# Kernel optimization log

Measured on AMD Instinct MI355X. Metric: run time of the kernel, lower is better.

Reference implementation:

```python
import jax, jax.numpy as jnp
import numpy as np

T, B, D, E, H = 64, 1024, 128, 256, 512


def _gru(x_emb, h0, W_ih, W_hh, b_ih, b_hh):
    """Standard GRU (PyTorch gate convention) over time-major x_emb [T,B,E]."""
    xW = x_emb @ W_ih + b_ih  # [T,B,3H], precompute input contractions

    def step(h, xw):
        hW = h @ W_hh + b_hh
        xr, xz, xn = jnp.split(xw, 3, axis=-1)
        hr, hz, hn = jnp.split(hW, 3, axis=-1)
        r = jax.nn.sigmoid(xr + hr)
        z = jax.nn.sigmoid(xz + hz)
        n = jnp.tanh(xn + r * hn)
        h_new = (1.0 - z) * n + z * h
        return h_new, h_new

    h_t, ys = jax.lax.scan(step, h0, xW)
    return ys, h_t


def setup_inputs() -> dict:
    key = jax.random.key(0)
    ks = jax.random.split(key, 16)
    s_in = 1.0 / np.sqrt(D)
    s_emb = 1.0 / np.sqrt(E)
    s_hid = 1.0 / np.sqrt(H)
    return {
        "past_input": jax.random.normal(ks[0], (T, B, D), jnp.float32),
        "future_input": jax.random.normal(ks[1], (T, B, D), jnp.float32),
        "noise": jax.random.normal(ks[2], (B, H), jnp.float32),
        "W_emb": jax.random.normal(ks[3], (D, E), jnp.float32) * s_in,
        "b_emb": jnp.zeros((E,), jnp.float32),
        "W_ih_enc": jax.random.normal(ks[4], (E, 3 * H), jnp.float32) * s_emb,
        "W_hh_enc": jax.random.normal(ks[5], (H, 3 * H), jnp.float32) * s_hid,
        "b_ih_enc": jnp.zeros((3 * H,), jnp.float32),
        "b_hh_enc": jnp.zeros((3 * H,), jnp.float32),
        "W_ih_dec": jax.random.normal(ks[6], (E, 3 * H), jnp.float32) * s_emb,
        "W_hh_dec": jax.random.normal(ks[7], (H, 3 * H), jnp.float32) * s_hid,
        "b_ih_dec": jnp.zeros((3 * H,), jnp.float32),
        "b_hh_dec": jnp.zeros((3 * H,), jnp.float32),
        "W_out": jax.random.normal(ks[8], (H, D), jnp.float32) * s_hid,
        "b_out": jnp.zeros((D,), jnp.float32),
    }


def reference(past_input, future_input, noise, W_emb, b_emb,
              W_ih_enc, W_hh_enc, b_ih_enc, b_hh_enc,
              W_ih_dec, W_hh_dec, b_ih_dec, b_hh_dec,
              W_out, b_out):
    past_emb = jax.nn.relu(past_input @ W_emb + b_emb)      # [T,B,E]
    fut_emb = jax.nn.relu(future_input @ W_emb + b_emb)     # [T,B,E]

    h0 = jnp.zeros((past_emb.shape[1], W_hh_enc.shape[0]), past_emb.dtype)
    _, h_t = _gru(past_emb, h0, W_ih_enc, W_hh_enc, b_ih_enc, b_hh_enc)

    # shift future embedding: step 0 -> zeros, step t -> emb at t-1
    fut_shift = jnp.concatenate([jnp.zeros_like(fut_emb[:1]), fut_emb[:-1]], axis=0)

    hidden = h_t + noise
    future_target, _ = _gru(fut_shift, hidden, W_ih_dec, W_hh_dec, b_ih_dec, b_hh_dec)
    return future_target @ W_out + b_out  # [T,B,D]
```

## Files before the change

### kernel.cpp

```cpp
#include <hip/hip_runtime.h>

typedef __bf16 bf16;
typedef __bf16 bf16x8 __attribute__((ext_vector_type(8)));
typedef float f32x4 __attribute__((ext_vector_type(4)));

#define Tt 64
#define Bb 1024
#define Dd 128
#define Ee 256
#define Hh 512
#define H3 1536

__device__ __forceinline__ float sigmf(float x) { return 1.0f / (1.0f + __expf(-x)); }
__device__ __forceinline__ float tanhfast(float x) {
    float e = __expf(2.0f * x);
    return 1.0f - 2.0f / (e + 1.0f);
}

#define LD_SC(dst, bp, OFF) \
    asm volatile("global_load_dwordx4 %0, %1, off offset:" #OFF " sc0 sc1" : "=v"(dst) : "v"(bp))
#define ST_SC(bp, OFF, val) \
    asm volatile("global_store_short %0, %1, off offset:" #OFF " sc0 sc1" :: "v"(bp), "v"(val))
#define LDROW16(arr, bp) \
    LD_SC(arr[0], bp, 0);    LD_SC(arr[1], bp, 64);   LD_SC(arr[2], bp, 128);  LD_SC(arr[3], bp, 192);  \
    LD_SC(arr[4], bp, 256);  LD_SC(arr[5], bp, 320);  LD_SC(arr[6], bp, 384);  LD_SC(arr[7], bp, 448);  \
    LD_SC(arr[8], bp, 512);  LD_SC(arr[9], bp, 576);  LD_SC(arr[10], bp, 640); LD_SC(arr[11], bp, 704); \
    LD_SC(arr[12], bp, 768); LD_SC(arr[13], bp, 832); LD_SC(arr[14], bp, 896); LD_SC(arr[15], bp, 960);

__global__ void k_prep(const float* __restrict__ We, const float* __restrict__ Wie, const float* __restrict__ Whe,
                       const float* __restrict__ Wid, const float* __restrict__ Whd, const float* __restrict__ Wo,
                       bf16* __restrict__ dWe, bf16* __restrict__ dWie, bf16* __restrict__ dWhe,
                       bf16* __restrict__ dWid, bf16* __restrict__ dWhd, bf16* __restrict__ dWo) {
    long i = (long)blockIdx.x * 256 + threadIdx.x;
    const float* s;
    bf16* d;
    int K, N;
    if (i < 32768) { s = We; d = dWe; K = Dd; N = Ee; }
    else if ((i -= 32768) < 393216) { s = Wie; d = dWie; K = Ee; N = H3; }
    else if ((i -= 393216) < 786432) { s = Whe; d = dWhe; K = Hh; N = H3; }
    else if ((i -= 786432) < 393216) { s = Wid; d = dWid; K = Ee; N = H3; }
    else if ((i -= 393216) < 786432) { s = Whd; d = dWhd; K = Hh; N = H3; }
    else if ((i -= 786432) < 65536) { s = Wo; d = dWo; K = Hh; N = Dd; }
    else return;
    int n = (int)(i / K), k = (int)(i - (long)n * K);
    d[i] = (bf16)s[(size_t)k * N + n];
}

__global__ __launch_bounds__(256) void k_embed(const float* __restrict__ xP, const float* __restrict__ xF,
                                               const bf16* __restrict__ WT, const float* __restrict__ bias,
                                               bf16* __restrict__ oP, bf16* __restrict__ oF) {
    const int lane = threadIdx.x & 63, wv = threadIdx.x >> 6;
    const float* x = blockIdx.z ? xF : xP;
    bf16* o = blockIdx.z ? oF : oP;
    const int m0w = blockIdx.x * 128 + wv * 32;
    const int c0 = blockIdx.y * 64;
    const int koff = (lane >> 4) * 8;
    f32x4 acc[2][4];
#pragma unroll
    for (int m = 0; m < 2; ++m)
#pragma unroll
        for (int s = 0; s < 4; ++s) acc[m][s] = f32x4{0.f, 0.f, 0.f, 0.f};

    const float* xp0 = x + (size_t)(m0w + (lane & 15)) * Dd + koff;
#pragma unroll
    for (int kc = 0; kc < 4; ++kc) {
        bf16x8 a0, a1;
        {
            float4 f0 = *(const float4*)(xp0 + kc * 32);
            float4 f1 = *(const float4*)(xp0 + kc * 32 + 4);
            a0[0] = (bf16)f0.x; a0[1] = (bf16)f0.y; a0[2] = (bf16)f0.z; a0[3] = (bf16)f0.w;
            a0[4] = (bf16)f1.x; a0[5] = (bf16)f1.y; a0[6] = (bf16)f1.z; a0[7] = (bf16)f1.w;
            float4 g0 = *(const float4*)(xp0 + 16 * Dd + kc * 32);
            float4 g1 = *(const float4*)(xp0 + 16 * Dd + kc * 32 + 4);
            a1[0] = (bf16)g0.x; a1[1] = (bf16)g0.y; a1[2] = (bf16)g0.z; a1[3] = (bf16)g0.w;
            a1[4] = (bf16)g1.x; a1[5] = (bf16)g1.y; a1[6] = (bf16)g1.z; a1[7] = (bf16)g1.w;
        }
#pragma unroll
        for (int s = 0; s < 4; ++s) {
            bf16x8 b = *(const bf16x8*)(WT + (size_t)(c0 + s * 16 + (lane & 15)) * Dd + kc * 32 + koff);
            acc[0][s] = __builtin_amdgcn_mfma_f32_16x16x32_bf16(a0, b, acc[0][s], 0, 0, 0);
            acc[1][s] = __builtin_amdgcn_mfma_f32_16x16x32_bf16(a1, b, acc[1][s], 0, 0, 0);
        }
    }
#pragma unroll
    for (int m = 0; m < 2; ++m)
#pragma unroll
        for (int s = 0; s < 4; ++s) {
            int col = c0 + s * 16 + (lane & 15);
            float bv = bias[col];
#pragma unroll
            for (int r = 0; r < 4; ++r) {
                int row = m0w + m * 16 + (lane >> 4) * 4 + r;
                o[(size_t)row * Ee + col] = (bf16)fmaxf(acc[m][s][r] + bv, 0.0f);
            }
        }
}

__global__ __launch_bounds__(256, 1) void k_gru_all(
    const bf16* __restrict__ embP, const bf16* __restrict__ embF, const float* __restrict__ noise,
    const bf16* __restrict__ WihE, const bf16* __restrict__ WhhE,
    const float* __restrict__ bIhE, const float* __restrict__ bHhE,
    const bf16* __restrict__ WihD, const bf16* __restrict__ WhhD,
    const float* __restrict__ bIhD, const float* __restrict__ bHhD,
    bf16* __restrict__ hA, bf16* __restrict__ hB, bf16* __restrict__ ys, unsigned* __restrict__ ctrs) {
    __shared__ bf16 Wih[6 * 8 * 64 * 8];
    __shared__ bf16 Whh[6 * 16 * 64 * 8];
    const int tid = threadIdx.x;
    const int lane = tid & 63, wv = tid >> 6;
    const int im = blockIdx.x >> 4;
    const int in = blockIdx.x & 15;
    const int rh = wv >> 1, ch = wv & 1;
    const int rowb = im * 64 + rh * 32;
    const int arow0 = rowb + (lane & 15);
    const int koff = (lane >> 4) * 8;
    const int colc = in * 32 + ch * 16 + (lane & 15);
    unsigned* ctr = ctrs + (size_t)im * 64;

    const bf16x8* WihV = (const bf16x8*)Wih;
    const bf16x8* WhhV = (const bf16x8*)Whh;

    auto stage = [&](const bf16* WT, int Kdim, int KC, bf16* lds) {
        int total = 6 * KC * 64;
        for (int idx = tid; idx < total; idx += 256) {
            int ln = idx & 63;
            int kc = (idx >> 6) % KC;
            int s = (idx >> 6) / KC;
            int gate = s >> 1, f = s & 1;
            int col = gate * Hh + in * 32 + f * 16 + (ln & 15);
            int k = kc * 32 + (ln >> 4) * 8;
            *(bf16x8*)(lds + (size_t)idx * 8) = *(const bf16x8*)(WT + (size_t)col * Kdim + k);
        }
    };

    float bi[3], bh[3];
    auto load_bias = [&](const float* bIh, const float* bHh) {
#pragma unroll
        for (int g = 0; g < 3; ++g) {
            bi[g] = bIh[g * Hh + colc];
            bh[g] = bHh[g * Hh + colc];
        }
    };

    auto signal = [&]() {
        asm volatile("s_waitcnt vmcnt(0)" ::: "memory");
        __syncthreads();
        if (tid == 0) atomicAdd(ctr, 1u);
    };
    auto wait_for = [&](unsigned target) {
        while (__hip_atomic_load(ctr, __ATOMIC_RELAXED, __HIP_MEMORY_SCOPE_AGENT) < target)
            __builtin_amdgcn_s_sleep(1);
    };

    f32x4 aR[2], aZ[2], aNX[2], aNH[2];
    auto zacc = [&]() {
#pragma unroll
        for (int i = 0; i < 2; ++i) {
            aR[i] = f32x4{0.f, 0.f, 0.f, 0.f};
            aZ[i] = f32x4{0.f, 0.f, 0.f, 0.f};
            aNX[i] = f32x4{0.f, 0.f, 0.f, 0.f};
            aNH[i] = f32x4{0.f, 0.f, 0.f, 0.f};
        }
    };

    auto xp_phase = [&](const bf16* xp) {
        const bf16* a0p = xp + (size_t)arow0 * Ee + koff;
#pragma unroll
        for (int kc = 0; kc < 8; ++kc) {
            bf16x8 a0 = *(const bf16x8*)(a0p + kc * 32);
            bf16x8 a1 = *(const bf16x8*)(a0p + 16 * Ee + kc * 32);
            bf16x8 br = WihV[((0 + ch) * 8 + kc) * 64 + lane];
            bf16x8 bz = WihV[((2 + ch) * 8 + kc) * 64 + lane];
            bf16x8 bn = WihV[((4 + ch) * 8 + kc) * 64 + lane];
            aR[0] = __builtin_amdgcn_mfma_f32_16x16x32_bf16(a0, br, aR[0], 0, 0, 0);
            aR[1] = __builtin_amdgcn_mfma_f32_16x16x32_bf16(a1, br, aR[1], 0, 0, 0);
            aZ[0] = __builtin_amdgcn_mfma_f32_16x16x32_bf16(a0, bz, aZ[0], 0, 0, 0);
            aZ[1] = __builtin_amdgcn_mfma_f32_16x16x32_bf16(a1, bz, aZ[1], 0, 0, 0);
            aNX[0] = __builtin_amdgcn_mfma_f32_16x16x32_bf16(a0, bn, aNX[0], 0, 0, 0);
            aNX[1] = __builtin_amdgcn_mfma_f32_16x16x32_bf16(a1, bn, aNX[1], 0, 0, 0);
        }
    };

    auto hw_phase = [&](const bf16* hp) {
        const bf16* h0p = hp + (size_t)arow0 * Hh + koff;
        const bf16* h1p = h0p + 16 * Hh;
        bf16x8 h0[16], h1[16];
        LDROW16(h0, h0p);
        LDROW16(h1, h1p);
        asm volatile("s_waitcnt vmcnt(0)" ::: "memory");
        __builtin_amdgcn_sched_barrier(0);
#pragma unroll
        for (int kc = 0; kc < 16; ++kc) {
            bf16x8 br = WhhV[((0 + ch) * 16 + kc) * 64 + lane];
            bf16x8 bz = WhhV[((2 + ch) * 16 + kc) * 64 + lane];
            bf16x8 bn = WhhV[((4 + ch) * 16 + kc) * 64 + lane];
            aR[0] = __builtin_amdgcn_mfma_f32_16x16x32_bf16(h0[kc], br, aR[0], 0, 0, 0);
            aR[1] = __builtin_amdgcn_mfma_f32_16x16x32_bf16(h1[kc], br, aR[1], 0, 0, 0);
            aZ[0] = __builtin_amdgcn_mfma_f32_16x16x32_bf16(h0[kc], bz, aZ[0], 0, 0, 0);
            aZ[1] = __builtin_amdgcn_mfma_f32_16x16x32_bf16(h1[kc], bz, aZ[1], 0, 0, 0);
            aNH[0] = __builtin_amdgcn_mfma_f32_16x16x32_bf16(h0[kc], bn, aNH[0], 0, 0, 0);
            aNH[1] = __builtin_amdgcn_mfma_f32_16x16x32_bf16(h1[kc], bn, aNH[1], 0, 0, 0);
        }
    };

    float hreg[8];
#pragma unroll
    for (int i = 0; i < 8; ++i) hreg[i] = 0.0f;

    auto epi = [&](bf16* op) {
#pragma unroll
        for (int rf = 0; rf < 2; ++rf) {
            bf16* stb = op + (size_t)(rowb + rf * 16 + (lane >> 4) * 4) * Hh + colc;
            unsigned short us[4];
#pragma unroll
            for (int r = 0; r < 4; ++r) {
                float rg = sigmf(aR[rf][r] + bi[0] + bh[0]);
                float zg = sigmf(aZ[rf][r] + bi[1] + bh[1]);
                float ng = tanhfast(aNX[rf][r] + bi[2] + rg * (aNH[rf][r] + bh[2]));
                float hv = (1.0f - zg) * ng + zg * hreg[rf * 4 + r];
                hreg[rf * 4 + r] = hv;
                us[r] = __builtin_bit_cast(unsigned short, (bf16)hv);
            }
            ST_SC(stb, 0, us[0]);
            ST_SC(stb, 1024, us[1]);
            ST_SC(stb, 2048, us[2]);
            ST_SC(stb, 3072, us[3]);
        }
    };

    stage(WihE, Ee, 8, Wih);
    stage(WhhE, Hh, 16, Whh);
    load_bias(bIhE, bHhE);
    __syncthreads();

#pragma unroll 1
    for (int t = 0; t < Tt; ++t) {
        zacc();
        xp_phase(embP + (size_t)t * Bb * Ee);
        if (t > 0) {
            wait_for(16u * t);
            hw_phase(((t - 1) & 1) ? hB : hA);
        }
        epi((t & 1) ? hB : hA);
        signal();
    }

    wait_for(16u * Tt);
    {
#pragma unroll
        for (int rf = 0; rf < 2; ++rf) {
            bf16* stb = hA + (size_t)(rowb + rf * 16 + (lane >> 4) * 4) * Hh + colc;
            unsigned short us[4];
#pragma unroll
            for (int r = 0; r < 4; ++r) {
                int row = rowb + rf * 16 + (lane >> 4) * 4 + r;
                float v = hreg[rf * 4 + r] + noise[(size_t)row * Hh + colc];
                hreg[rf * 4 + r] = v;
                us[r] = __builtin_bit_cast(unsigned short, (bf16)v);
            }
            ST_SC(stb, 0, us[0]);
            ST_SC(stb, 1024, us[1]);
            ST_SC(stb, 2048, us[2]);
            ST_SC(stb, 3072, us[3]);
        }
    }
    stage(WihD, Ee, 8, Wih);
    stage(WhhD, Hh, 16, Whh);
    load_bias(bIhD, bHhD);
    signal();
    wait_for(16u * (Tt + 1));

#pragma unroll 1
    for (int t = 0; t < Tt; ++t) {
        zacc();
        if (t > 0) {
            xp_phase(embF + (size_t)(t - 1) * Bb * Ee);
            wait_for(16u * (Tt + 1 + t));
        }
        hw_phase(t ? ys + (size_t)(t - 1) * Bb * Hh : hA);
        epi(ys + (size_t)t * Bb * Hh);
        if (t < Tt - 1) signal();
    }
}

__global__ __launch_bounds__(256) void k_out(const bf16* __restrict__ ys, const bf16* __restrict__ WT,
                                             const float* __restrict__ bias, float* __restrict__ out) {
    const int lane = threadIdx.x & 63, wv = threadIdx.x >> 6;
    const int m0w = blockIdx.x * 256 + wv * 64;
    const int c0 = blockIdx.y * 64;
    const int koff = (lane >> 4) * 8;
    f32x4 acc[4][4];
#pragma unroll
    for (int m = 0; m < 4; ++m)
#pragma unroll
        for (int s = 0; s < 4; ++s) acc[m][s] = f32x4{0.f, 0.f, 0.f, 0.f};

    const bf16* ap = ys + (size_t)(m0w + (lane & 15)) * Hh + koff;
#pragma unroll
    for (int kc = 0; kc < 16; ++kc) {
        bf16x8 a0 = *(const bf16x8*)(ap + kc * 32);
        bf16x8 a1 = *(const bf16x8*)(ap + 16 * Hh + kc * 32);
        bf16x8 a2 = *(const bf16x8*)(ap + 32 * Hh + kc * 32);
        bf16x8 a3 = *(const bf16x8*)(ap + 48 * Hh + kc * 32);
#pragma unroll
        for (int s = 0; s < 4; ++s) {
            bf16x8 b = *(const bf16x8*)(WT + (size_t)(c0 + s * 16 + (lane & 15)) * Hh + kc * 32 + koff);
            acc[0][s] = __builtin_amdgcn_mfma_f32_16x16x32_bf16(a0, b, acc[0][s], 0, 0, 0);
            acc[1][s] = __builtin_amdgcn_mfma_f32_16x16x32_bf16(a1, b, acc[1][s], 0, 0, 0);
            acc[2][s] = __builtin_amdgcn_mfma_f32_16x16x32_bf16(a2, b, acc[2][s], 0, 0, 0);
            acc[3][s] = __builtin_amdgcn_mfma_f32_16x16x32_bf16(a3, b, acc[3][s], 0, 0, 0);
        }
    }
#pragma unroll
    for (int m = 0; m < 4; ++m)
#pragma unroll
        for (int s = 0; s < 4; ++s) {
            int col = c0 + s * 16 + (lane & 15);
            float bv = bias[col];
#pragma unroll
            for (int r = 0; r < 4; ++r) {
                int row = m0w + m * 16 + (lane >> 4) * 4 + r;
                out[(size_t)row * Dd + col] = acc[m][s][r] + bv;
            }
        }
}

extern "C" void kernel_launch(void* const* d_in, const int* in_sizes, int n_in,
                              void* d_out, int out_size, void* d_ws, size_t ws_size,
                              hipStream_t stream) {
    const float* past = (const float*)d_in[0];
    const float* fut = (const float*)d_in[1];
    const float* noise = (const float*)d_in[2];
    const float* W_emb = (const float*)d_in[3];
    const float* b_emb = (const float*)d_in[4];
    const float* W_ih_enc = (const float*)d_in[5];
    const float* W_hh_enc = (const float*)d_in[6];
    const float* b_ih_enc = (const float*)d_in[7];
    const float* b_hh_enc = (const float*)d_in[8];
    const float* W_ih_dec = (const float*)d_in[9];
    const float* W_hh_dec = (const float*)d_in[10];
    const float* b_ih_dec = (const float*)d_in[11];
    const float* b_hh_dec = (const float*)d_in[12];
    const float* W_out = (const float*)d_in[13];
    const float* b_out = (const float*)d_in[14];
    float* out = (float*)d_out;

    char* w = (char*)d_ws;
    auto alloc = [&](size_t bytes) {
        char* p = w;
        w += (bytes + 255) & ~(size_t)255;
        return p;
    };
    bf16* embP = (bf16*)alloc((size_t)Tt * Bb * Ee * 2);
    bf16* embF = (bf16*)alloc((size_t)Tt * Bb * Ee * 2);
    bf16* ys = (bf16*)alloc((size_t)Tt * Bb * Hh * 2);
    bf16* hA = (bf16*)alloc((size_t)Bb * Hh * 2);
    bf16* hB = (bf16*)alloc((size_t)Bb * Hh * 2);
    bf16* WembT = (bf16*)alloc((size_t)Ee * Dd * 2);
    bf16* WihEncT = (bf16*)alloc((size_t)H3 * Ee * 2);
    bf16* WhhEncT = (bf16*)alloc((size_t)H3 * Hh * 2);
    bf16* WihDecT = (bf16*)alloc((size_t)H3 * Ee * 2);
    bf16* WhhDecT = (bf16*)alloc((size_t)H3 * Hh * 2);
    bf16* WoutT = (bf16*)alloc((size_t)Dd * Hh * 2);
    unsigned* ctrs = (unsigned*)alloc(16 * 64 * sizeof(unsigned));

    k_prep<<<9600, 256, 0, stream>>>(W_emb, W_ih_enc, W_hh_enc, W_ih_dec, W_hh_dec, W_out,
                                     WembT, WihEncT, WhhEncT, WihDecT, WhhDecT, WoutT);

    k_embed<<<dim3(Tt * Bb / 128, Ee / 64, 2), 256, 0, stream>>>(past, fut, WembT, b_emb, embP, embF);

    hipMemsetAsync(ctrs, 0, 16 * 64 * sizeof(unsigned), stream);

    void* args[] = {(void*)&embP, (void*)&embF, (void*)&noise,
                    (void*)&WihEncT, (void*)&WhhEncT, (void*)&b_ih_enc, (void*)&b_hh_enc,
                    (void*)&WihDecT, (void*)&WhhDecT, (void*)&b_ih_dec, (void*)&b_hh_dec,
                    (void*)&hA, (void*)&hB, (void*)&ys, (void*)&ctrs};
    hipLaunchCooperativeKernel((const void*)k_gru_all, dim3(256), dim3(256), args, 0, stream);

    k_out<<<dim3(Tt * Bb / 256, Dd / 64), 256, 0, stream>>>(ys, WoutT, b_out, out);
}
```

Measured before the change: 1.226 ms.

## Double GRU block to 512 threads and replace atomic counter with per-block flags

```diff
diff --git a/kernel.cpp b/kernel.cpp
--- a/kernel.cpp
+++ b/kernel.cpp
@@ -96,13 +96,13 @@
         }
 }
 
-__global__ __launch_bounds__(256, 1) void k_gru_all(
+__global__ __launch_bounds__(512, 1) void k_gru_all(
     const bf16* __restrict__ embP, const bf16* __restrict__ embF, const float* __restrict__ noise,
     const bf16* __restrict__ WihE, const bf16* __restrict__ WhhE,
     const float* __restrict__ bIhE, const float* __restrict__ bHhE,
     const bf16* __restrict__ WihD, const bf16* __restrict__ WhhD,
     const float* __restrict__ bIhD, const float* __restrict__ bHhD,
-    bf16* __restrict__ hA, bf16* __restrict__ hB, bf16* __restrict__ ys, unsigned* __restrict__ ctrs) {
+    bf16* __restrict__ hA, bf16* __restrict__ hB, bf16* __restrict__ ys, unsigned* __restrict__ flags) {
     __shared__ bf16 Wih[6 * 8 * 64 * 8];
     __shared__ bf16 Whh[6 * 16 * 64 * 8];
     const int tid = threadIdx.x;
@@ -110,18 +110,17 @@
     const int im = blockIdx.x >> 4;
     const int in = blockIdx.x & 15;
     const int rh = wv >> 1, ch = wv & 1;
-    const int rowb = im * 64 + rh * 32;
+    const int rowb = im * 64 + rh * 16;
     const int arow0 = rowb + (lane & 15);
     const int koff = (lane >> 4) * 8;
     const int colc = in * 32 + ch * 16 + (lane & 15);
-    unsigned* ctr = ctrs + (size_t)im * 64;
 
     const bf16x8* WihV = (const bf16x8*)Wih;
     const bf16x8* WhhV = (const bf16x8*)Whh;
 
     auto stage = [&](const bf16* WT, int Kdim, int KC, bf16* lds) {
         int total = 6 * KC * 64;
-        for (int idx = tid; idx < total; idx += 256) {
+        for (int idx = tid; idx < total; idx += 512) {
             int ln = idx & 63;
             int kc = (idx >> 6) % KC;
             int s = (idx >> 6) / KC;
@@ -141,90 +140,78 @@
         }
     };
 
-    auto signal = [&]() {
+    auto signal = [&](unsigned seq) {
         asm volatile("s_waitcnt vmcnt(0)" ::: "memory");
         __syncthreads();
-        if (tid == 0) atomicAdd(ctr, 1u);
-    };
-    auto wait_for = [&](unsigned target) {
-        while (__hip_atomic_load(ctr, __ATOMIC_RELAXED, __HIP_MEMORY_SCOPE_AGENT) < target)
+        if (tid == 0) {
+            unsigned* fp = flags + ((size_t)im * 16 + in) * 16;
+            asm volatile("global_store_dword %0, %1, off sc0 sc1" :: "v"(fp), "v"(seq) : "memory");
+        }
+    };
+    auto wait_flags = [&](unsigned seq) {
+        const unsigned* fp = flags + ((size_t)im * 16 + (lane & 15)) * 16;
+        for (;;) {
+            unsigned v;
+            asm volatile("global_load_dword %0, %1, off sc0 sc1\n\ts_waitcnt vmcnt(0)"
+                         : "=v"(v) : "v"(fp) : "memory");
+            if (__all((int)(v >= seq))) break;
             __builtin_amdgcn_s_sleep(1);
-    };
-
-    f32x4 aR[2], aZ[2], aNX[2], aNH[2];
+        }
+    };
+
+    f32x4 aR, aZ, aNX, aNH;
     auto zacc = [&]() {
-#pragma unroll
-        for (int i = 0; i < 2; ++i) {
-            aR[i] = f32x4{0.f, 0.f, 0.f, 0.f};
-            aZ[i] = f32x4{0.f, 0.f, 0.f, 0.f};
-            aNX[i] = f32x4{0.f, 0.f, 0.f, 0.f};
-            aNH[i] = f32x4{0.f, 0.f, 0.f, 0.f};
-        }
+        aR = f32x4{0.f, 0.f, 0.f, 0.f};
+        aZ = f32x4{0.f, 0.f, 0.f, 0.f};
+        aNX = f32x4{0.f, 0.f, 0.f, 0.f};
+        aNH = f32x4{0.f, 0.f, 0.f, 0.f};
     };
 
     auto xp_phase = [&](const bf16* xp) {
-        const bf16* a0p = xp + (size_t)arow0 * Ee + koff;
+        const bf16* ap = xp + (size_t)arow0 * Ee + koff;
 #pragma unroll
         for (int kc = 0; kc < 8; ++kc) {
-            bf16x8 a0 = *(const bf16x8*)(a0p + kc * 32);
-            bf16x8 a1 = *(const bf16x8*)(a0p + 16 * Ee + kc * 32);
-            bf16x8 br = WihV[((0 + ch) * 8 + kc) * 64 + lane];
-            bf16x8 bz = WihV[((2 + ch) * 8 + kc) * 64 + lane];
-            bf16x8 bn = WihV[((4 + ch) * 8 + kc) * 64 + lane];
-            aR[0] = __builtin_amdgcn_mfma_f32_16x16x32_bf16(a0, br, aR[0], 0, 0, 0);
-            aR[1] = __builtin_amdgcn_mfma_f32_16x16x32_bf16(a1, br, aR[1], 0, 0, 0);
-            aZ[0] = __builtin_amdgcn_mfma_f32_16x16x32_bf16(a0, bz, aZ[0], 0, 0, 0);
-            aZ[1] = __builtin_amdgcn_mfma_f32_16x16x32_bf16(a1, bz, aZ[1], 0, 0, 0);
-            aNX[0] = __builtin_amdgcn_mfma_f32_16x16x32_bf16(a0, bn, aNX[0], 0, 0, 0);
-            aNX[1] = __builtin_amdgcn_mfma_f32_16x16x32_bf16(a1, bn, aNX[1], 0, 0, 0);
+            bf16x8 a = *(const bf16x8*)(ap + kc * 32);
+            aR = __builtin_amdgcn_mfma_f32_16x16x32_bf16(a, WihV[((0 + ch) * 8 + kc) * 64 + lane], aR, 0, 0, 0);
+            aZ = __builtin_amdgcn_mfma_f32_16x16x32_bf16(a, WihV[((2 + ch) * 8 + kc) * 64 + lane], aZ, 0, 0, 0);
+            aNX = __builtin_amdgcn_mfma_f32_16x16x32_bf16(a, WihV[((4 + ch) * 8 + kc) * 64 + lane], aNX, 0, 0, 0);
         }
     };
 
     auto hw_phase = [&](const bf16* hp) {
         const bf16* h0p = hp + (size_t)arow0 * Hh + koff;
-        const bf16* h1p = h0p + 16 * Hh;
-        bf16x8 h0[16], h1[16];
+        bf16x8 h0[16];
         LDROW16(h0, h0p);
-        LDROW16(h1, h1p);
         asm volatile("s_waitcnt vmcnt(0)" ::: "memory");
         __builtin_amdgcn_sched_barrier(0);
 #pragma unroll
         for (int kc = 0; kc < 16; ++kc) {
-            bf16x8 br = WhhV[((0 + ch) * 16 + kc) * 64 + lane];
-            bf16x8 bz = WhhV[((2 + ch) * 16 + kc) * 64 + lane];
-            bf16x8 bn = WhhV[((4 + ch) * 16 + kc) * 64 + lane];
-            aR[0] = __builtin_amdgcn_mfma_f32_16x16x32_bf16(h0[kc], br, aR[0], 0, 0, 0);
-            aR[1] = __builtin_amdgcn_mfma_f32_16x16x32_bf16(h1[kc], br, aR[1], 0, 0, 0);
-            aZ[0] = __builtin_amdgcn_mfma_f32_16x16x32_bf16(h0[kc], bz, aZ[0], 0, 0, 0);
-            aZ[1] = __builtin_amdgcn_mfma_f32_16x16x32_bf16(h1[kc], bz, aZ[1], 0, 0, 0);
-            aNH[0] = __builtin_amdgcn_mfma_f32_16x16x32_bf16(h0[kc], bn, aNH[0], 0, 0, 0);
-            aNH[1] = __builtin_amdgcn_mfma_f32_16x16x32_bf16(h1[kc], bn, aNH[1], 0, 0, 0);
-        }
-    };
-
-    float hreg[8];
-#pragma unroll
-    for (int i = 0; i < 8; ++i) hreg[i] = 0.0f;
+            aR = __builtin_amdgcn_mfma_f32_16x16x32_bf16(h0[kc], WhhV[((0 + ch) * 16 + kc) * 64 + lane], aR, 0, 0, 0);
+            aZ = __builtin_amdgcn_mfma_f32_16x16x32_bf16(h0[kc], WhhV[((2 + ch) * 16 + kc) * 64 + lane], aZ, 0, 0, 0);
+            aNH = __builtin_amdgcn_mfma_f32_16x16x32_bf16(h0[kc], WhhV[((4 + ch) * 16 + kc) * 64 + lane], aNH, 0, 0, 0);
+        }
+    };
+
+    float hreg[4];
+#pragma unroll
+    for (int i = 0; i < 4; ++i) hreg[i] = 0.0f;
 
     auto epi = [&](bf16* op) {
-#pragma unroll
-        for (int rf = 0; rf < 2; ++rf) {
-            bf16* stb = op + (size_t)(rowb + rf * 16 + (lane >> 4) * 4) * Hh + colc;
-            unsigned short us[4];
-#pragma unroll
-            for (int r = 0; r < 4; ++r) {
-                float rg = sigmf(aR[rf][r] + bi[0] + bh[0]);
-                float zg = sigmf(aZ[rf][r] + bi[1] + bh[1]);
-                float ng = tanhfast(aNX[rf][r] + bi[2] + rg * (aNH[rf][r] + bh[2]));
-                float hv = (1.0f - zg) * ng + zg * hreg[rf * 4 + r];
-                hreg[rf * 4 + r] = hv;
-                us[r] = __builtin_bit_cast(unsigned short, (bf16)hv);
-            }
-            ST_SC(stb, 0, us[0]);
-            ST_SC(stb, 1024, us[1]);
-            ST_SC(stb, 2048, us[2]);
-            ST_SC(stb, 3072, us[3]);
-        }
+        bf16* stb = op + (size_t)(rowb + (lane >> 4) * 4) * Hh + colc;
+        unsigned short us[4];
+#pragma unroll
+        for (int r = 0; r < 4; ++r) {
+            float rg = sigmf(aR[r] + bi[0] + bh[0]);
+            float zg = sigmf(aZ[r] + bi[1] + bh[1]);
+            float ng = tanhfast(aNX[r] + bi[2] + rg * (aNH[r] + bh[2]));
+            float hv = (1.0f - zg) * ng + zg * hreg[r];
+            hreg[r] = hv;
+            us[r] = __builtin_bit_cast(unsigned short, (bf16)hv);
+        }
+        ST_SC(stb, 0, us[0]);
+        ST_SC(stb, 1024, us[1]);
+        ST_SC(stb, 2048, us[2]);
+        ST_SC(stb, 3072, us[3]);
     };
 
     stage(WihE, Ee, 8, Wih);
@@ -237,48 +224,45 @@
         zacc();
         xp_phase(embP + (size_t)t * Bb * Ee);
         if (t > 0) {
-            wait_for(16u * t);
+            wait_flags((unsigned)t);
             hw_phase(((t - 1) & 1) ? hB : hA);
         }
         epi((t & 1) ? hB : hA);
-        signal();
-    }
-
-    wait_for(16u * Tt);
+        signal((unsigned)(t + 1));
+    }
+
+    wait_flags((unsigned)Tt);
     {
-#pragma unroll
-        for (int rf = 0; rf < 2; ++rf) {
-            bf16* stb = hA + (size_t)(rowb + rf * 16 + (lane >> 4) * 4) * Hh + colc;
-            unsigned short us[4];
-#pragma unroll
-            for (int r = 0; r < 4; ++r) {
-                int row = rowb + rf * 16 + (lane >> 4) * 4 + r;
-                float v = hreg[rf * 4 + r] + noise[(size_t)row * Hh + colc];
-                hreg[rf * 4 + r] = v;
-                us[r] = __builtin_bit_cast(unsigned short, (bf16)v);
-            }
-            ST_SC(stb, 0, us[0]);
-            ST_SC(stb, 1024, us[1]);
-            ST_SC(stb, 2048, us[2]);
-            ST_SC(stb, 3072, us[3]);
-        }
+        bf16* stb = hA + (size_t)(rowb + (lane >> 4) * 4) * Hh + colc;
+        unsigned short us[4];
+#pragma unroll
+        for (int r = 0; r < 4; ++r) {
+            int row = rowb + (lane >> 4) * 4 + r;
+            float v = hreg[r] + noise[(size_t)row * Hh + colc];
+            hreg[r] = v;
+            us[r] = __builtin_bit_cast(unsigned short, (bf16)v);
+        }
+        ST_SC(stb, 0, us[0]);
+        ST_SC(stb, 1024, us[1]);
+        ST_SC(stb, 2048, us[2]);
+        ST_SC(stb, 3072, us[3]);
     }
     stage(WihD, Ee, 8, Wih);
     stage(WhhD, Hh, 16, Whh);
     load_bias(bIhD, bHhD);
-    signal();
-    wait_for(16u * (Tt + 1));
+    signal((unsigned)(Tt + 1));
+    wait_flags((unsigned)(Tt + 1));
 
 #pragma unroll 1
     for (int t = 0; t < Tt; ++t) {
         zacc();
         if (t > 0) {
             xp_phase(embF + (size_t)(t - 1) * Bb * Ee);
-            wait_for(16u * (Tt + 1 + t));
+            wait_flags((unsigned)(Tt + 1 + t));
         }
         hw_phase(t ? ys + (size_t)(t - 1) * Bb * Hh : hA);
         epi(ys + (size_t)t * Bb * Hh);
-        if (t < Tt - 1) signal();
+        if (t < Tt - 1) signal((unsigned)(Tt + 2 + t));
     }
 }
 
@@ -361,20 +345,20 @@
     bf16* WihDecT = (bf16*)alloc((size_t)H3 * Ee * 2);
     bf16* WhhDecT = (bf16*)alloc((size_t)H3 * Hh * 2);
     bf16* WoutT = (bf16*)alloc((size_t)Dd * Hh * 2);
-    unsigned* ctrs = (unsigned*)alloc(16 * 64 * sizeof(unsigned));
+    unsigned* flags = (unsigned*)alloc(16 * 16 * 64);
 
     k_prep<<<9600, 256, 0, stream>>>(W_emb, W_ih_enc, W_hh_enc, W_ih_dec, W_hh_dec, W_out,
                                      WembT, WihEncT, WhhEncT, WihDecT, WhhDecT, WoutT);
 
     k_embed<<<dim3(Tt * Bb / 128, Ee / 64, 2), 256, 0, stream>>>(past, fut, WembT, b_emb, embP, embF);
 
-    hipMemsetAsync(ctrs, 0, 16 * 64 * sizeof(unsigned), stream);
+    hipMemsetAsync(flags, 0, 16 * 16 * 64, stream);
 
     void* args[] = {(void*)&embP, (void*)&embF, (void*)&noise,
                     (void*)&WihEncT, (void*)&WhhEncT, (void*)&b_ih_enc, (void*)&b_hh_enc,
                     (void*)&WihDecT, (void*)&WhhDecT, (void*)&b_ih_dec, (void*)&b_hh_dec,
-                    (void*)&hA, (void*)&hB, (void*)&ys, (void*)&ctrs};
-    hipLaunchCooperativeKernel((const void*)k_gru_all, dim3(256), dim3(256), args, 0, stream);
+                    (void*)&hA, (void*)&hB, (void*)&ys, (void*)&flags};
+    hipLaunchCooperativeKernel((const void*)k_gru_all, dim3(256), dim3(512), args, 0, stream);
 
     k_out<<<dim3(Tt * Bb / 256, Dd / 64), 256, 0, stream>>>(ys, WoutT, b_out, out);
 }
```

After: 1.096 ms. 10.6% less time.

## Replace per-row-group atomic counter with per-wave flags and progressive h loading

Applied to the files above, without the earlier changes.

```diff
diff --git a/kernel.cpp b/kernel.cpp
--- a/kernel.cpp
+++ b/kernel.cpp
@@ -18,14 +18,9 @@
 }
 
 #define LD_SC(dst, bp, OFF) \
-    asm volatile("global_load_dwordx4 %0, %1, off offset:" #OFF " sc0 sc1" : "=v"(dst) : "v"(bp))
+    asm volatile("global_load_dwordx4 %0, %1, off offset:" #OFF " sc1" : "=&v"(dst) : "v"(bp))
 #define ST_SC(bp, OFF, val) \
-    asm volatile("global_store_short %0, %1, off offset:" #OFF " sc0 sc1" :: "v"(bp), "v"(val))
-#define LDROW16(arr, bp) \
-    LD_SC(arr[0], bp, 0);    LD_SC(arr[1], bp, 64);   LD_SC(arr[2], bp, 128);  LD_SC(arr[3], bp, 192);  \
-    LD_SC(arr[4], bp, 256);  LD_SC(arr[5], bp, 320);  LD_SC(arr[6], bp, 384);  LD_SC(arr[7], bp, 448);  \
-    LD_SC(arr[8], bp, 512);  LD_SC(arr[9], bp, 576);  LD_SC(arr[10], bp, 640); LD_SC(arr[11], bp, 704); \
-    LD_SC(arr[12], bp, 768); LD_SC(arr[13], bp, 832); LD_SC(arr[14], bp, 896); LD_SC(arr[15], bp, 960);
+    asm volatile("global_store_short %0, %1, off offset:" #OFF " sc1" :: "v"(bp), "v"(val))
 
 __global__ void k_prep(const float* __restrict__ We, const float* __restrict__ Wie, const float* __restrict__ Whe,
                        const float* __restrict__ Wid, const float* __restrict__ Whd, const float* __restrict__ Wo,
@@ -102,19 +97,21 @@
     const float* __restrict__ bIhE, const float* __restrict__ bHhE,
     const bf16* __restrict__ WihD, const bf16* __restrict__ WhhD,
     const float* __restrict__ bIhD, const float* __restrict__ bHhD,
-    bf16* __restrict__ hA, bf16* __restrict__ hB, bf16* __restrict__ ys, unsigned* __restrict__ ctrs) {
+    bf16* __restrict__ hA, bf16* __restrict__ hB, bf16* __restrict__ ys, unsigned* __restrict__ flags) {
     __shared__ bf16 Wih[6 * 8 * 64 * 8];
     __shared__ bf16 Whh[6 * 16 * 64 * 8];
     const int tid = threadIdx.x;
     const int lane = tid & 63, wv = tid >> 6;
-    const int im = blockIdx.x >> 4;
-    const int in = blockIdx.x & 15;
+    const int bid = blockIdx.x;
+    const int im = (bid & 7) * 2 + (bid >> 7);
+    const int in = (bid >> 3) & 15;
     const int rh = wv >> 1, ch = wv & 1;
     const int rowb = im * 64 + rh * 32;
     const int arow0 = rowb + (lane & 15);
     const int koff = (lane >> 4) * 8;
     const int colc = in * 32 + ch * 16 + (lane & 15);
-    unsigned* ctr = ctrs + (size_t)im * 64;
+    unsigned* dom = flags + ((size_t)im * 2 + rh) * 32 * 16;
+    const int myidx = in * 2 + ch;
 
     const bf16x8* WihV = (const bf16x8*)Wih;
     const bf16x8* WhhV = (const bf16x8*)Whh;
@@ -141,14 +138,22 @@
         }
     };
 
-    auto signal = [&]() {
+    auto signal = [&](unsigned seq) {
         asm volatile("s_waitcnt vmcnt(0)" ::: "memory");
-        __syncthreads();
-        if (tid == 0) atomicAdd(ctr, 1u);
-    };
-    auto wait_for = [&](unsigned target) {
-        while (__hip_atomic_load(ctr, __ATOMIC_RELAXED, __HIP_MEMORY_SCOPE_AGENT) < target)
-            __builtin_amdgcn_s_sleep(1);
+        if (lane == 0) {
+            unsigned* fp = dom + myidx * 16;
+            asm volatile("global_store_dword %0, %1, off sc1" :: "v"(fp), "v"(seq) : "memory");
+        }
+    };
+    auto poll = [&](unsigned seq) -> unsigned long long {
+        unsigned v;
+        const unsigned* fp = dom + (lane & 31) * 16;
+        asm volatile("global_load_dword %0, %1, off sc1\n\ts_waitcnt vmcnt(0)"
+                     : "=&v"(v) : "v"(fp) : "memory");
+        return __ballot((int)(v >= seq));
+    };
+    auto wait_all = [&](unsigned seq) {
+        while (poll(seq) != ~0ULL) __builtin_amdgcn_s_sleep(2);
     };
 
     f32x4 aR[2], aZ[2], aNX[2], aNH[2];
@@ -180,12 +185,20 @@
         }
     };
 
-    auto hw_phase = [&](const bf16* hp) {
+    auto hw_phase = [&](const bf16* hp, unsigned seq) {
         const bf16* h0p = hp + (size_t)arow0 * Hh + koff;
         const bf16* h1p = h0p + 16 * Hh;
         bf16x8 h0[16], h1[16];
-        LDROW16(h0, h0p);
-        LDROW16(h1, h1p);
+        unsigned long long rdy = poll(seq);
+#define HSTEP(p, OFF) \
+        while (((rdy >> (2 * p)) & 3ULL) != 3ULL) { __builtin_amdgcn_s_sleep(2); rdy = poll(seq); } \
+        LD_SC(h0[p], h0p, OFF); \
+        LD_SC(h1[p], h1p, OFF);
+        HSTEP(0, 0)    HSTEP(1, 64)   HSTEP(2, 128)  HSTEP(3, 192)
+        HSTEP(4, 256)  HSTEP(5, 320)  HSTEP(6, 384)  HSTEP(7, 448)
+        HSTEP(8, 512)  HSTEP(9, 576)  HSTEP(10, 640) HSTEP(11, 704)
+        HSTEP(12, 768) HSTEP(13, 832) HSTEP(14, 896) HSTEP(15, 960)
+#undef HSTEP
         asm volatile("s_waitcnt vmcnt(0)" ::: "memory");
         __builtin_amdgcn_sched_barrier(0);
 #pragma unroll
@@ -236,15 +249,12 @@
     for (int t = 0; t < Tt; ++t) {
         zacc();
         xp_phase(embP + (size_t)t * Bb * Ee);
-        if (t > 0) {
-            wait_for(16u * t);
-            hw_phase(((t - 1) & 1) ? hB : hA);
-        }
+        if (t > 0) hw_phase(((t - 1) & 1) ? hB : hA, (unsigned)t);
         epi((t & 1) ? hB : hA);
-        signal();
-    }
-
-    wait_for(16u * Tt);
+        signal((unsigned)(t + 1));
+    }
+
+    wait_all((unsigned)Tt);
     {
 #pragma unroll
         for (int rf = 0; rf < 2; ++rf) {
@@ -263,22 +273,20 @@
             ST_SC(stb, 3072, us[3]);
         }
     }
+    __syncthreads();
     stage(WihD, Ee, 8, Wih);
     stage(WhhD, Hh, 16, Whh);
+    __syncthreads();
     load_bias(bIhD, bHhD);
-    signal();
-    wait_for(16u * (Tt + 1));
+    signal((unsigned)(Tt + 1));
 
 #pragma unroll 1
     for (int t = 0; t < Tt; ++t) {
         zacc();
-        if (t > 0) {
-            xp_phase(embF + (size_t)(t - 1) * Bb * Ee);
-            wait_for(16u * (Tt + 1 + t));
-        }
-        hw_phase(t ? ys + (size_t)(t - 1) * Bb * Hh : hA);
+        if (t > 0) xp_phase(embF + (size_t)(t - 1) * Bb * Ee);
+        hw_phase(t ? ys + (size_t)(t - 1) * Bb * Hh : hA, (unsigned)(Tt + 1 + t));
         epi(ys + (size_t)t * Bb * Hh);
-        if (t < Tt - 1) signal();
+        if (t < Tt - 1) signal((unsigned)(Tt + 2 + t));
     }
 }
 
@@ -361,19 +369,19 @@
     bf16* WihDecT = (bf16*)alloc((size_t)H3 * Ee * 2);
     bf16* WhhDecT = (bf16*)alloc((size_t)H3 * Hh * 2);
     bf16* WoutT = (bf16*)alloc((size_t)Dd * Hh * 2);
-    unsigned* ctrs = (unsigned*)alloc(16 * 64 * sizeof(unsigned));
+    unsigned* flags = (unsigned*)alloc(16 * 2 * 32 * 16 * sizeof(unsigned));
 
     k_prep<<<9600, 256, 0, stream>>>(W_emb, W_ih_enc, W_hh_enc, W_ih_dec, W_hh_dec, W_out,
                                      WembT, WihEncT, WhhEncT, WihDecT, WhhDecT, WoutT);
 
     k_embed<<<dim3(Tt * Bb / 128, Ee / 64, 2), 256, 0, stream>>>(past, fut, WembT, b_emb, embP, embF);
 
-    hipMemsetAsync(ctrs, 0, 16 * 64 * sizeof(unsigned), stream);
+    hipMemsetAsync(flags, 0, 16 * 2 * 32 * 16 * sizeof(unsigned), stream);
 
     void* args[] = {(void*)&embP, (void*)&embF, (void*)&noise,
                     (void*)&WihEncT, (void*)&WhhEncT, (void*)&b_ih_enc, (void*)&b_hh_enc,
                     (void*)&WihDecT, (void*)&WhhDecT, (void*)&b_ih_dec, (void*)&b_hh_dec,
-                    (void*)&hA, (void*)&hB, (void*)&ys, (void*)&ctrs};
+                    (void*)&hA, (void*)&hB, (void*)&ys, (void*)&flags};
     hipLaunchCooperativeKernel((const void*)k_gru_all, dim3(256), dim3(256), args, 0, stream);
 
     k_out<<<dim3(Tt * Bb / 256, Dd / 64), 256, 0, stream>>>(ys, WoutT, b_out, out);
```

After: 1.108 ms. 9.6% less time.
